# Performance work log

Hardware: AMD Instinct MI355X
Metric: run time of the kernel (lower is better)

Reference implementation:

```python
import math
import jax, jax.numpy as jnp
import numpy as np

LOG_K = 9          # log_kernel_size
SIGMA_MIN = 0.5
SIGMA_MAX = 10.0


def setup_inputs() -> dict:
    key = jax.random.key(0)
    k1, k2 = jax.random.split(key)
    B, C, H, W = 4, 3, 256, 256
    x = jax.random.normal(k1, (B, C, H, W), dtype=jnp.float32)
    # foa_xy holds (x, y) pixel coordinates of the focus of attention
    foa_xy = jax.random.uniform(k2, (B, 2), dtype=jnp.float32) * jnp.array([W - 1, H - 1], jnp.float32)
    return {"x": x, "foa_xy": foa_xy}


def _log_per_pixel_kernels(foa_xy, H, W, k, sigma_min, sigma_max):
    """Per-pixel LoG kernels, shape [B, k*k, H*W] (out_ch=in_ch=1 spatial-only)."""
    B = foa_xy.shape[0]
    kk = k * k
    # pixel coordinate grid (x, y), flattened row-major: [HW, 2]
    yy, xx = jnp.meshgrid(jnp.arange(H), jnp.arange(W), indexing="ij")
    xx_yy = jnp.stack([xx.ravel(), yy.ravel()], axis=-1).astype(jnp.float32)
    # squared distances within the kernel window: [kk]
    r = jnp.arange(-(k // 2), k // 2 + 1)
    ryy, rxx = jnp.meshgrid(r, r, indexing="ij")
    r_sq = (rxx ** 2 + ryy ** 2).reshape(-1).astype(jnp.float32)
    # distance of every pixel from the FOA: [B, HW]
    diff = xx_yy[None, :, :] - foa_xy[:, None, :]
    dists = jnp.sqrt(jnp.sum(diff ** 2, axis=-1))
    diag = math.sqrt(H * H + W * W)
    dn = dists / diag
    sigma = (1.0 - dn) * sigma_min + dn * sigma_max        # linear sigma, [B, HW]
    s = sigma[:, None, :]                                   # [B, 1, HW]
    tmp = r_sq[None, :, None] / (2.0 * s * s)               # [B, kk, HW]
    factor = -1.0 / (math.pi * s ** 4)
    kern = factor * (1.0 - tmp) * jnp.exp(-tmp)
    kern = kern * jnp.sqrt(s)                               # scale_factor = sigma**0.5
    kern = kern * dists[:, None, :]                         # distance modulation
    return kern                                             # [B, kk, HW]


def reference(x, foa_xy):
    B, C, H, W = x.shape
    k = LOG_K
    pad = ((k - 1) * 1 + 1) // 2                            # dilation=1 -> 4
    xp = jnp.pad(x, ((0, 0), (0, 0), (pad, pad), (pad, pad)), mode="reflect")
    # im2col: [B, C*kk, H, W], feature dim ordered (channel-major, then kernel pos)
    patches = jax.lax.conv_general_dilated_patches(xp, (k, k), (1, 1), "VALID")
    patches = patches.reshape(B, C, k * k, H * W)
    kern = _log_per_pixel_kernels(foa_xy, H, W, k, SIGMA_MIN, SIGMA_MAX)  # [B, kk, HW]
    # spatial-only kernel: sum over kernel-area dim, broadcast over channels
    out = jnp.einsum("bckp,bkp->bcp", patches, kern)
    return out.reshape(B, C, H, W)
```

## Files before the change

kernel.cpp:

```cpp
#include <hip/hip_runtime.h>
#include <math.h>

#define HH 256
#define WW 256
#define CC 3
#define HW (HH*WW)

#define PW 272
#define PH 264
#define PIMG (PH*PW)

__device__ __forceinline__ int reflect(int v, int n) {
    v = (v < 0) ? -v : v;
    v = (v > n - 1) ? (2 * (n - 1) - v) : v;
    return v;
}

__device__ __forceinline__ constexpr int r2idx(int r2) {
    switch (r2) {
        case 0:  return 0;  case 1:  return 1;  case 2:  return 2;  case 4:  return 3;
        case 5:  return 4;  case 8:  return 5;  case 9:  return 6;  case 10: return 7;
        case 13: return 8;  case 16: return 9;  case 17: return 10; case 18: return 11;
        case 20: return 12; case 25: return 13; case 26: return 14; default: return 15;
    }
}

__global__ __launch_bounds__(256) void pad_kernel(
    const float* __restrict__ x, float* __restrict__ pw)
{
    const int row = blockIdx.x;
    const int bc  = row / PH;
    const int r   = row - bc * PH;
    const int gr  = reflect(r - 4, HH);
    const float* src = x + (size_t)bc * HW + gr * WW;
    float* dst = pw + (size_t)row * PW;
    for (int i = threadIdx.x; i < PW; i += 256) {
        int gc = i - 4;
        gc = (gc < 0) ? -gc : gc;
        gc = (gc > WW - 1) ? (2 * (WW - 1) - gc) : gc;
        dst[i] = src[gc];
    }
}

__global__ __launch_bounds__(128) void adaptive_log_kernel(
    const float* __restrict__ pin, const float* __restrict__ foa,
    float* __restrict__ out)
{
    const int tid  = threadIdx.x;
    const int lane = tid & 63;
    const int x0   = lane * 4;
    const int y    = blockIdx.x * 2 + (tid >> 6);
    const int b    = blockIdx.y;

    const float fx = foa[2 * b + 0];
    const float fy = foa[2 * b + 1];
    float w[4][16];
    #pragma unroll
    for (int o = 0; o < 4; ++o) {
        const float ddx = (float)(x0 + o) - fx;
        const float ddy = (float)y - fy;
        const float dist = sqrtf(ddx * ddx + ddy * ddy);
        const float dn = dist * (1.0f / 362.03867196751236f);
        const float sigma = 0.5f + 9.5f * dn;
        const float s2 = sigma * sigma;
        const float inv2s2 = 0.5f / s2;
        const float common = (-1.0f / (float)M_PI) / (s2 * s2) * sqrtf(sigma) * dist;
        const float q   = __expf(-inv2s2);
        const float q2  = q * q;
        const float q4  = q2 * q2;
        const float q5  = q4 * q;
        const float q8  = q4 * q4;
        const float q16 = q8 * q8;
        const float ee[16]  = {1.0f, q, q2, q4, q5, q8, q8*q, q8*q2, q8*q5,
                               q16, q16*q, q16*q2, q16*q4, q16*q8*q, q16*q8*q2, q16*q16};
        const float r2v[16] = {0,1,2,4,5,8,9,10,13,16,17,18,20,25,26,32};
        const float cb = common * inv2s2;
        #pragma unroll
        for (int k = 0; k < 16; ++k)
            w[o][k] = (common - r2v[k] * cb) * ee[k];
    }

    float acc[CC][4] = {};
    const float* basep = pin + (size_t)b * (CC * PIMG) + x0;
    #pragma unroll
    for (int c = 0; c < CC; ++c) {
        const float* cp = basep + c * PIMG;
        #pragma unroll
        for (int i = 0; i < 9; ++i) {
            const float4* rp = (const float4*)(cp + (y + i) * PW);
            const float4 A = rp[0];
            const float4 B = rp[1];
            const float4 C4 = rp[2];
            const float f[12] = {A.x,A.y,A.z,A.w, B.x,B.y,B.z,B.w, C4.x,C4.y,C4.z,C4.w};
            const int dy2 = (i - 4) * (i - 4);
            #pragma unroll
            for (int o = 0; o < 4; ++o) {
                float s = 0.f;
                #pragma unroll
                for (int m = 0; m < 9; ++m)
                    s += w[o][r2idx(dy2 + (m - 4) * (m - 4))] * f[o + m];
                acc[c][o] += s;
            }
        }
    }

    float* ob = out + (size_t)b * (CC * HW) + y * WW + x0;
    #pragma unroll
    for (int c = 0; c < CC; ++c)
        *(float4*)&ob[c * HW] = make_float4(acc[c][0], acc[c][1], acc[c][2], acc[c][3]);
}

extern "C" void kernel_launch(void* const* d_in, const int* in_sizes, int n_in,
                              void* d_out, int out_size, void* d_ws, size_t ws_size,
                              hipStream_t stream) {
    const float* x   = (const float*)d_in[0];
    const float* foa = (const float*)d_in[1];
    float* out = (float*)d_out;
    float* pw  = (float*)d_ws;

    pad_kernel<<<dim3(4 * CC * PH), dim3(256), 0, stream>>>(x, pw);

    adaptive_log_kernel<<<dim3(HH / 2, 4), dim3(128), 0, stream>>>(pw, foa, out);
}
```

Baseline: 78.49 us.

## Split channels across waves, pad only columns, and vectorize the pad copy

The pad kernel now pads only horizontally, using one wave per row with float4 copies plus a few reflected edge writes. Vertical reflection moves into the main kernel through precomputed row offsets. The main kernel gives each wave a single (channel, row) instead of all three channels, which triples the number of waves and cuts accumulator registers, using 256-thread blocks with an occupancy hint. In exchange, each wave recomputes the per-pixel LoG weights, so that arithmetic now runs three times as often.

After: 83.24 us. 1.06x slower.

```diff
diff --git a/kernel.cpp b/kernel.cpp
--- a/kernel.cpp
+++ b/kernel.cpp
@@ -5,10 +5,8 @@
 #define WW 256
 #define CC 3
 #define HW (HH*WW)
-
-#define PW 272
-#define PH 264
-#define PIMG (PH*PW)
+#define PW 264
+#define NROWS (4*CC*HH)
 
 __device__ __forceinline__ int reflect(int v, int n) {
     v = (v < 0) ? -v : v;
@@ -28,29 +26,34 @@
 __global__ __launch_bounds__(256) void pad_kernel(
     const float* __restrict__ x, float* __restrict__ pw)
 {
-    const int row = blockIdx.x;
-    const int bc  = row / PH;
-    const int r   = row - bc * PH;
-    const int gr  = reflect(r - 4, HH);
-    const float* src = x + (size_t)bc * HW + gr * WW;
+    const int row  = blockIdx.x * 4 + (threadIdx.x >> 6);
+    const int lane = threadIdx.x & 63;
+    const float* src = x + (size_t)row * WW;
     float* dst = pw + (size_t)row * PW;
-    for (int i = threadIdx.x; i < PW; i += 256) {
-        int gc = i - 4;
-        gc = (gc < 0) ? -gc : gc;
-        gc = (gc > WW - 1) ? (2 * (WW - 1) - gc) : gc;
-        dst[i] = src[gc];
+    *(float4*)(dst + 4 + lane * 4) = *(const float4*)(src + lane * 4);
+    if (lane < 8) {
+        const int i = (lane < 4) ? lane : (256 + lane);
+        dst[i] = src[reflect(i - 4, WW)];
     }
 }
 
-__global__ __launch_bounds__(128) void adaptive_log_kernel(
+__global__ __launch_bounds__(256, 3) void adaptive_log_kernel(
     const float* __restrict__ pin, const float* __restrict__ foa,
     float* __restrict__ out)
 {
     const int tid  = threadIdx.x;
     const int lane = tid & 63;
     const int x0   = lane * 4;
-    const int y    = blockIdx.x * 2 + (tid >> 6);
+    const int gw   = blockIdx.x * 4 + (tid >> 6);
+    const int c    = gw >> 8;
+    const int y    = gw & 255;
     const int b    = blockIdx.y;
+
+    const float* base = pin + (size_t)((b * CC + c) * HH) * PW + x0;
+    int ro[9];
+    #pragma unroll
+    for (int i = 0; i < 9; ++i)
+        ro[i] = reflect(y + i - 4, HH) * PW;
 
     const float fx = foa[2 * b + 0];
     const float fy = foa[2 * b + 1];
@@ -80,34 +83,27 @@
             w[o][k] = (common - r2v[k] * cb) * ee[k];
     }
 
-    float acc[CC][4] = {};
-    const float* basep = pin + (size_t)b * (CC * PIMG) + x0;
+    float acc[4] = {0.f, 0.f, 0.f, 0.f};
     #pragma unroll
-    for (int c = 0; c < CC; ++c) {
-        const float* cp = basep + c * PIMG;
+    for (int i = 0; i < 9; ++i) {
+        const float* rp = base + ro[i];
+        const float4 A = *(const float4*)(rp);
+        const float4 B = *(const float4*)(rp + 4);
+        const float4 C4 = *(const float4*)(rp + 8);
+        const float f[12] = {A.x,A.y,A.z,A.w, B.x,B.y,B.z,B.w, C4.x,C4.y,C4.z,C4.w};
+        const int dy2 = (i - 4) * (i - 4);
         #pragma unroll
-        for (int i = 0; i < 9; ++i) {
-            const float4* rp = (const float4*)(cp + (y + i) * PW);
-            const float4 A = rp[0];
-            const float4 B = rp[1];
-            const float4 C4 = rp[2];
-            const float f[12] = {A.x,A.y,A.z,A.w, B.x,B.y,B.z,B.w, C4.x,C4.y,C4.z,C4.w};
-            const int dy2 = (i - 4) * (i - 4);
+        for (int o = 0; o < 4; ++o) {
+            float s = 0.f;
             #pragma unroll
-            for (int o = 0; o < 4; ++o) {
-                float s = 0.f;
-                #pragma unroll
-                for (int m = 0; m < 9; ++m)
-                    s += w[o][r2idx(dy2 + (m - 4) * (m - 4))] * f[o + m];
-                acc[c][o] += s;
-            }
+            for (int m = 0; m < 9; ++m)
+                s += w[o][r2idx(dy2 + (m - 4) * (m - 4))] * f[o + m];
+            acc[o] += s;
         }
     }
 
-    float* ob = out + (size_t)b * (CC * HW) + y * WW + x0;
-    #pragma unroll
-    for (int c = 0; c < CC; ++c)
-        *(float4*)&ob[c * HW] = make_float4(acc[c][0], acc[c][1], acc[c][2], acc[c][3]);
+    float* ob = out + (size_t)(b * CC + c) * HW + y * WW + x0;
+    *(float4*)ob = make_float4(acc[0], acc[1], acc[2], acc[3]);
 }
 
 extern "C" void kernel_launch(void* const* d_in, const int* in_sizes, int n_in,
@@ -118,7 +114,6 @@
     float* out = (float*)d_out;
     float* pw  = (float*)d_ws;
 
-    pad_kernel<<<dim3(4 * CC * PH), dim3(256), 0, stream>>>(x, pw);
-
-    adaptive_log_kernel<<<dim3(HH / 2, 4), dim3(128), 0, stream>>>(pw, foa, out);
+    pad_kernel<<<dim3(NROWS / 4), dim3(256), 0, stream>>>(x, pw);
+    adaptive_log_kernel<<<dim3(192, 4), dim3(256), 0, stream>>>(pw, foa, out);
 }
```
